# Performance work log

Hardware: AMD Instinct MI355X
Metric: run time of the kernel (lower is better)

## Reference

```python
import jax, jax.numpy as jnp
import numpy as np

NUM_EMB = 256
EMB_DIM = 32
B, N = 16, 16384
TEMPERATURE = 1.0      # current value of the temperature buffer
TEMP_MIN = 0.5
TEMP_INIT_REF = 2.0    # constant used in temp_ratio denominator in the torch code


def setup_inputs() -> dict:
    key = jax.random.key(0)
    k1, k2, k3 = jax.random.split(key, 3)
    inputs = jax.random.normal(k1, (B, N, EMB_DIM), dtype=jnp.float32)
    embedding = jax.random.normal(k2, (NUM_EMB, EMB_DIM), dtype=jnp.float32) * 0.1
    gumbel_u = jax.random.uniform(k3, (B * N, NUM_EMB), dtype=jnp.float32)
    return {"inputs": inputs, "embedding": embedding, "gumbel_u": gumbel_u}


def reference(inputs, embedding, gumbel_u):
    input_shape = inputs.shape
    flat = inputs.reshape(-1, EMB_DIM)                       # [M, D]

    distances = (jnp.sum(flat ** 2, axis=1, keepdims=True)
                 - 2.0 * jnp.matmul(flat, embedding.T)
                 + jnp.sum(embedding ** 2, axis=1))
    logits = -distances / TEMPERATURE

    # training branch: gumbel noise + softmax at temperature
    gumbel = -jnp.log(-jnp.log(gumbel_u + 1e-20) + 1e-20)
    soft = jax.nn.softmax((logits + gumbel) / TEMPERATURE, axis=-1)  # [M, K]

    quantized_soft = jnp.matmul(soft, embedding)             # [M, D]
    indices = jnp.argmax(soft, axis=-1)                      # [M]
    quantized_hard = embedding[indices]                      # [M, D]

    temp_ratio = (TEMPERATURE - TEMP_MIN) / (TEMP_INIT_REF - TEMP_MIN)
    quantized = temp_ratio * quantized_soft + (1.0 - temp_ratio) * quantized_hard
    # straight-through estimator
    quantized = flat + jax.lax.stop_gradient(quantized - flat)

    commitment_loss = jnp.mean((jax.lax.stop_gradient(quantized_hard) - flat) ** 2)

    avg_probs = jnp.mean(soft, axis=0)                       # [K]
    perplexity = jnp.exp(-jnp.sum(avg_probs * jnp.log(avg_probs + 1e-10)))

    quantized = quantized.reshape(input_shape)
    indices = indices.reshape(input_shape[:-1])
    return quantized, commitment_loss, indices, perplexity
```

## Files before the change

kernel.cpp:

```cpp
#include <hip/hip_runtime.h>


#define M_ROWS  262144
#define OUT_LOSS 8388608
#define OUT_IDX  8388609
#define OUT_PPL  8650753

#if defined(__has_builtin)
#if __has_builtin(__builtin_amdgcn_global_load_lds)
#define HAVE_GLLDS 1
#else
#define HAVE_GLLDS 0
#endif
#else
#define HAVE_GLLDS 0
#endif

typedef float f32x2 __attribute__((ext_vector_type(2)));

__device__ __forceinline__ f32x2 mk2(float a, float b) {
  f32x2 r; r.x = a; r.y = b; return r;
}

__device__ __forceinline__ unsigned int f2bf_u(float f) {
  unsigned int u = __float_as_uint(f);
  u += 0x7fffu + ((u >> 16) & 1u);
  return u >> 16;
}
__device__ __forceinline__ float bf2f(unsigned int lo16) {
  return __uint_as_float(lo16 << 16);
}

__global__ __launch_bounds__(256) void vq_prep(const float* __restrict__ emb,
                                               float* __restrict__ ws) {
  int t = threadIdx.x;
  ws[t] = 0.0f;
  if (t == 0) ws[256] = 0.0f;
  const float4* e4 = (const float4*)emb;
  float s = 0.0f;
#pragma unroll
  for (int j = 0; j < 8; ++j) {
    float4 v = e4[t * 8 + j];
    s += v.x * v.x + v.y * v.y + v.z * v.z + v.w * v.w;
  }
  ws[257 + t] = s;
}

__global__ __launch_bounds__(256, 4) void vq_pass1(
    const float* __restrict__ x_in, const float* __restrict__ emb,
    const float* __restrict__ gum,
    float* __restrict__ invS_ws, unsigned short* __restrict__ p_ws,
    float* __restrict__ loss_ws, float* __restrict__ out) {
  __shared__ __align__(16) float x_lds[16 * 36];
  __shared__ __align__(16) float g_lds[16 * 256];
  __shared__ float t_lds[256 * 17];
  __shared__ float red_sum[16 * 17];
  __shared__ float red_max[16 * 17];
  __shared__ int   red_idx[16 * 17];

  const int tid = threadIdx.x;
  const int wv  = tid >> 6;
  const int ln  = tid & 63;

  const float S2    = 2.8853900817779268f;
  const float L2E   = 1.4426950408889634f;
  const float GOFF  = 0.5287663729448977f;
  const float EPS2  = 1.4426950408889634e-20f;

  f32x2 er2[16];
  float ne_t;
  {
    const float4* e4 = (const float4*)(emb + tid * 32);
    float na = 0.0f;
#pragma unroll
    for (int j = 0; j < 8; ++j) {
      float4 v = e4[j];
      na = fmaf(v.x, v.x, na); na = fmaf(v.y, v.y, na);
      na = fmaf(v.z, v.z, na); na = fmaf(v.w, v.w, na);
      er2[2*j]   = mk2(v.x * S2, v.y * S2);
      er2[2*j+1] = mk2(v.z * S2, v.w * S2);
    }
    ne_t = na * L2E;
  }
  const int row_blk = blockIdx.x * 256;
  float cl_acc = 0.0f;

#if HAVE_GLLDS
  auto issue_g = [&](int ttn) {
    const char* gbase = (const char*)(gum + (size_t)(row_blk + ttn * 16) * 256);
#pragma unroll
    for (int i = 0; i < 4; ++i) {
      const int off = i * 4096 + wv * 1024;
      __builtin_amdgcn_global_load_lds(
          (const __attribute__((address_space(1))) void*)(gbase + off + ln * 16),
          (__attribute__((address_space(3))) void*)((char*)g_lds + off),
          16, 0, 0);
    }
  };
  issue_g(0);
#endif

  for (int tt = 0; tt < 16; ++tt) {
    const int r0 = row_blk + tt * 16;

#if !HAVE_GLLDS
    {
      const float4* gg = (const float4*)gum + (size_t)r0 * 64;
      float4* gd = (float4*)g_lds;
#pragma unroll
      for (int i = 0; i < 4; ++i) gd[i * 256 + tid] = gg[i * 256 + tid];
    }
#endif
    if (tid < 128)
      *((float4*)&x_lds[(tid >> 3) * 36 + (tid & 7) * 4]) =
          ((const float4*)x_in)[(size_t)r0 * 8 + tid];
    __syncthreads();

#pragma unroll 1
    for (int r = 0; r < 16; ++r) {
      const float u = g_lds[r * 256 + tid];
      const float L1 = __log2f(u + 1e-20f);
      const float gp = GOFF - __log2f(EPS2 - L1);
      const float4* xr4 = (const float4*)&x_lds[r * 36];
      f32x2 a0 = mk2(0.f, 0.f), a1 = mk2(0.f, 0.f);
#pragma unroll
      for (int j = 0; j < 8; ++j) {
        const float4 xv = xr4[j];
        a0 = __builtin_elementwise_fma(mk2(xv.x, xv.y), er2[2*j],   a0);
        a1 = __builtin_elementwise_fma(mk2(xv.z, xv.w), er2[2*j+1], a1);
      }
      const float dot2 = (a0.x + a1.x) + (a0.y + a1.y);
      t_lds[tid * 17 + r] = dot2 + (gp - ne_t);
    }
    __syncthreads();

#if HAVE_GLLDS
    if (tt < 15) issue_g(tt + 1);
#endif

    const int lrow = tid & 15;
    const int cs   = tid >> 4;
    {
      float ssum = 0.0f, tmax = -3.0e38f;
      int   kmax = 0;
      unsigned int packs[8];
#pragma unroll
      for (int j = 0; j < 16; ++j) {
        const int k = cs * 16 + j;
        const float tv = t_lds[k * 17 + lrow];
        const float p = exp2f(tv);
        ssum += p;
        if (tv > tmax) { tmax = tv; kmax = k; }
        if (j & 1) packs[j >> 1] |= f2bf_u(p) << 16;
        else       packs[j >> 1]  = f2bf_u(p);
      }
      uint4* pout = (uint4*)(p_ws + (size_t)(r0 + lrow) * 256 + cs * 16);
      const uint4* pd = (const uint4*)packs;
      pout[0] = pd[0]; pout[1] = pd[1];
      red_sum[lrow * 17 + cs] = ssum;
      red_max[lrow * 17 + cs] = tmax;
      red_idx[lrow * 17 + cs] = kmax;
    }
    __syncthreads();

    if (tid < 16) {
      float ssum = 0.0f, tmax = -3.0e38f;
      int   kmax = 0;
#pragma unroll
      for (int c = 0; c < 16; ++c) {
        ssum += red_sum[tid * 17 + c];
        const float m = red_max[tid * 17 + c];
        if (m > tmax) { tmax = m; kmax = red_idx[tid * 17 + c]; }
      }
      const int rg = r0 + tid;
      invS_ws[rg] = 1.0f / ssum;
      out[OUT_IDX + rg] = (float)kmax;

      const float4* eh = (const float4*)(emb + (size_t)kmax * 32);
      const float* xrr = &x_lds[tid * 36];
      float cl = 0.0f;
#pragma unroll
      for (int j = 0; j < 8; ++j) {
        const float4 e  = eh[j];
        const float4 xv = ((const float4*)xrr)[j];
        float dx;
        dx = e.x - xv.x; cl = fmaf(dx, dx, cl);
        dx = e.y - xv.y; cl = fmaf(dx, dx, cl);
        dx = e.z - xv.z; cl = fmaf(dx, dx, cl);
        dx = e.w - xv.w; cl = fmaf(dx, dx, cl);
      }
#pragma unroll
      for (int off = 8; off > 0; off >>= 1) cl += __shfl_down(cl, off, 16);
      if (tid == 0) cl_acc += cl;
    }
    __syncthreads();
  }
  if (tid == 0) atomicAdd(loss_ws, cl_acc);
}

__global__ __launch_bounds__(256, 4) void vq_pass2(
    const float* __restrict__ emb, const unsigned short* __restrict__ p_ws,
    const float* __restrict__ invS_ws, float* __restrict__ out) {
  __shared__ __align__(16) float e_lds[256 * 32];

  const int tid = threadIdx.x;
  {
    const float4* src = (const float4*)emb;
    float4* dst = (float4*)e_lds;
#pragma unroll
    for (int j = 0; j < 8; ++j) dst[j * 256 + tid] = src[j * 256 + tid];
  }
  __syncthreads();

  const int row = blockIdx.x * 256 + tid;
  const float invS = invS_ws[row];
  const int imax = (int)out[OUT_IDX + row];
  const uint4* pv = (const uint4*)(p_ws + (size_t)row * 256);
  const float4* el4 = (const float4*)e_lds;

  f32x2 q2[16];
#pragma unroll
  for (int d = 0; d < 16; ++d) q2[d] = mk2(0.f, 0.f);

  for (int kg = 0; kg < 8; ++kg) {
    unsigned int w_[16];
#pragma unroll
    for (int j = 0; j < 4; ++j) {
      const uint4 v = pv[kg * 4 + j];
      w_[4*j+0] = v.x; w_[4*j+1] = v.y; w_[4*j+2] = v.z; w_[4*j+3] = v.w;
    }
#pragma unroll
    for (int i = 0; i < 16; ++i) {
      const int k0 = kg * 32 + 2 * i;
      const f32x2 pp0 = mk2(bf2f(w_[i] & 0xffffu), bf2f(w_[i] & 0xffffu));
      const f32x2 pp1 = mk2(bf2f(w_[i] >> 16),     bf2f(w_[i] >> 16));
#pragma unroll
      for (int jj = 0; jj < 8; ++jj) {
        const float4 e0 = el4[k0 * 8 + jj];
        const float4 e1 = el4[(k0 + 1) * 8 + jj];
        q2[2*jj]   = __builtin_elementwise_fma(mk2(e0.x, e0.y), pp0, q2[2*jj]);
        q2[2*jj+1] = __builtin_elementwise_fma(mk2(e0.z, e0.w), pp0, q2[2*jj+1]);
        q2[2*jj]   = __builtin_elementwise_fma(mk2(e1.x, e1.y), pp1, q2[2*jj]);
        q2[2*jj+1] = __builtin_elementwise_fma(mk2(e1.z, e1.w), pp1, q2[2*jj+1]);
      }
    }
  }

  const float tr  = 1.0f / 3.0f;
  const float otr = 1.0f - tr;
  const float4* ehv = el4 + imax * 8;
  float4* outq = (float4*)(out + (size_t)row * 32);
#pragma unroll
  for (int j = 0; j < 8; ++j) {
    float4 e = ehv[j];
    float4 o;
    o.x = fmaf(tr, q2[2*j].x   * invS, otr * e.x);
    o.y = fmaf(tr, q2[2*j].y   * invS, otr * e.y);
    o.z = fmaf(tr, q2[2*j+1].x * invS, otr * e.z);
    o.w = fmaf(tr, q2[2*j+1].y * invS, otr * e.w);
    outq[j] = o;
  }
}

__global__ __launch_bounds__(256) void vq_avg(
    const unsigned short* __restrict__ p_ws, const float* __restrict__ invS_ws,
    float* __restrict__ avg_ws) {
  __shared__ float sh[256];
  const int tid = threadIdx.x, lane = tid & 63, w = tid >> 6;
  sh[tid] = 0.0f;
  __syncthreads();
  const int base = (blockIdx.x * 4 + w) * 64;
  const float iv = invS_ws[base + lane];
  float a0 = 0.f, a1 = 0.f, a2 = 0.f, a3 = 0.f;
  for (int r = 0; r < 64; ++r) {
    const float s = __shfl(iv, r);
    const uint2 u2 = ((const uint2*)(p_ws + (size_t)(base + r) * 256))[lane];
    a0 = fmaf(bf2f(u2.x & 0xffffu), s, a0);
    a1 = fmaf(bf2f(u2.x >> 16),     s, a1);
    a2 = fmaf(bf2f(u2.y & 0xffffu), s, a2);
    a3 = fmaf(bf2f(u2.y >> 16),     s, a3);
  }
  atomicAdd(&sh[4*lane+0], a0);
  atomicAdd(&sh[4*lane+1], a1);
  atomicAdd(&sh[4*lane+2], a2);
  atomicAdd(&sh[4*lane+3], a3);
  __syncthreads();
  atomicAdd(&avg_ws[tid], sh[tid]);
}

__global__ __launch_bounds__(256) void vq_fin(const float* __restrict__ ws,
                                              float* __restrict__ out) {
  __shared__ float red[256];
  int t = threadIdx.x;
  float avg = ws[t] * (1.0f / 262144.0f);
  red[t] = -avg * __logf(avg + 1e-10f);
  __syncthreads();
  for (int s = 128; s > 0; s >>= 1) {
    if (t < s) red[t] += red[t + s];
    __syncthreads();
  }
  if (t == 0) {
    out[OUT_PPL]  = __expf(red[0]);
    out[OUT_LOSS] = ws[256] * (1.0f / 8388608.0f);
  }
}

__global__ __launch_bounds__(256, 1) void vq_main(
    const float* __restrict__ x_in, const float* __restrict__ emb,
    const float* __restrict__ gum, const float* __restrict__ ne,
    float* __restrict__ avg_ws, float* __restrict__ loss_ws,
    float* __restrict__ out) {
  extern __shared__ unsigned char dynsmem[];
  unsigned short* p_lds = (unsigned short*)dynsmem;

  const int tid  = threadIdx.x;
  const int lane = tid & 63;
  const int w    = tid >> 6;
  const int row  = blockIdx.x * 256 + tid;
  unsigned short* my_p = p_lds + (size_t)(w * 64 + lane) * 258;

  float xr[32];
  {
    const float4* xv = (const float4*)(x_in + (size_t)row * 32);
#pragma unroll
    for (int j = 0; j < 8; ++j) {
      float4 v = xv[j];
      xr[4*j+0] = v.x; xr[4*j+1] = v.y; xr[4*j+2] = v.z; xr[4*j+3] = v.w;
    }
  }
  float q[32];
#pragma unroll
  for (int d = 0; d < 32; ++d) q[d] = 0.0f;

  float ssum = 0.0f;
  float tmax = -3.0e38f;
  int   imax = 0;

  const float4* g4 = (const float4*)(gum + (size_t)row * 256);
  const float4* e4 = (const float4*)emb;

  for (int kg = 0; kg < 8; ++kg) {
    float uv[32];
#pragma unroll
    for (int j = 0; j < 8; ++j) {
      float4 v = g4[kg * 8 + j];
      uv[4*j+0] = v.x; uv[4*j+1] = v.y; uv[4*j+2] = v.z; uv[4*j+3] = v.w;
    }
#pragma unroll
    for (int kk = 0; kk < 32; ++kk) {
      const int k = kg * 32 + kk;
      float er[32];
#pragma unroll
      for (int j = 0; j < 8; ++j) {
        float4 v = e4[k * 8 + j];
        er[4*j+0] = v.x; er[4*j+1] = v.y; er[4*j+2] = v.z; er[4*j+3] = v.w;
      }
      float d0 = 0.f, d1 = 0.f, d2 = 0.f, d3 = 0.f;
#pragma unroll
      for (int d = 0; d < 32; d += 4) {
        d0 = fmaf(xr[d+0], er[d+0], d0);
        d1 = fmaf(xr[d+1], er[d+1], d1);
        d2 = fmaf(xr[d+2], er[d+2], d2);
        d3 = fmaf(xr[d+3], er[d+3], d3);
      }
      const float dot = (d0 + d1) + (d2 + d3);
      const float inner = -__logf(uv[kk] + 1e-20f);
      const float g = -__logf(inner + 1e-20f);
      const float t = fmaf(2.0f, dot, g) - ne[k];
      const float p = __expf(t);
      ssum += p;
      if (t > tmax) { tmax = t; imax = k; }
#pragma unroll
      for (int d = 0; d < 32; ++d) q[d] = fmaf(p, er[d], q[d]);
      my_p[k] = (unsigned short)f2bf_u(p);
    }
  }

  const float invS = 1.0f / ssum;
  {
    const float tr  = 1.0f / 3.0f;
    const float otr = 1.0f - tr;
    const float4* ehv = (const float4*)(emb + (size_t)imax * 32);
    float4* outq = (float4*)(out + (size_t)row * 32);
    float cl = 0.0f;
#pragma unroll
    for (int j = 0; j < 8; ++j) {
      float4 e = ehv[j];
      float4 o;
      float qs, dx;
      qs = q[4*j+0]*invS; o.x = tr*qs + otr*e.x; dx = e.x - xr[4*j+0]; cl = fmaf(dx,dx,cl);
      qs = q[4*j+1]*invS; o.y = tr*qs + otr*e.y; dx = e.y - xr[4*j+1]; cl = fmaf(dx,dx,cl);
      qs = q[4*j+2]*invS; o.z = tr*qs + otr*e.z; dx = e.z - xr[4*j+2]; cl = fmaf(dx,dx,cl);
      qs = q[4*j+3]*invS; o.w = tr*qs + otr*e.w; dx = e.w - xr[4*j+3]; cl = fmaf(dx,dx,cl);
      outq[j] = o;
    }
    out[OUT_IDX + row] = (float)imax;
#pragma unroll
    for (int off = 32; off > 0; off >>= 1) cl += __shfl_down(cl, off);
    if (lane == 0) atomicAdd(loss_ws, cl);
  }

  __syncthreads();

  float a0 = 0.f, a1 = 0.f, a2 = 0.f, a3 = 0.f;
  for (int r = 0; r < 64; ++r) {
    const float invS_r = __shfl(invS, r);
    const unsigned short* rp = p_lds + (size_t)(w * 64 + r) * 258;
    a0 = fmaf(bf2f(rp[  0 + lane]), invS_r, a0);
    a1 = fmaf(bf2f(rp[ 64 + lane]), invS_r, a1);
    a2 = fmaf(bf2f(rp[128 + lane]), invS_r, a2);
    a3 = fmaf(bf2f(rp[192 + lane]), invS_r, a3);
  }
  atomicAdd(&avg_ws[  0 + lane], a0);
  atomicAdd(&avg_ws[ 64 + lane], a1);
  atomicAdd(&avg_ws[128 + lane], a2);
  atomicAdd(&avg_ws[192 + lane], a3);
}

extern "C" void kernel_launch(void* const* d_in, const int* in_sizes, int n_in,
                              void* d_out, int out_size, void* d_ws, size_t ws_size,
                              hipStream_t stream) {
  const float* x   = (const float*)d_in[0];
  const float* emb = (const float*)d_in[1];
  const float* gum = (const float*)d_in[2];
  float* out = (float*)d_out;
  float* ws  = (float*)d_ws;

  (void)in_sizes; (void)n_in; (void)out_size;

  vq_prep<<<1, 256, 0, stream>>>(emb, ws);

  const size_t need = (size_t)(1024 + M_ROWS) * 4 + (size_t)M_ROWS * 256 * 2;
  if (ws_size >= need) {
    float* invS = ws + 1024;
    unsigned short* p = (unsigned short*)(ws + 1024 + M_ROWS);
    vq_pass1<<<1024, 256, 0, stream>>>(x, emb, gum, invS, p, ws + 256, out);
    vq_pass2<<<1024, 256, 0, stream>>>(emb, p, invS, out);
    vq_avg<<<1024, 256, 0, stream>>>(p, invS, ws);
  } else {
    (void)hipFuncSetAttribute((const void*)vq_main,
                        hipFuncAttributeMaxDynamicSharedMemorySize, 132128);
    vq_main<<<1024, 256, 132128, stream>>>(x, emb, gum, ws + 257, ws, ws + 256, out);
  }
  vq_fin<<<1, 256, 0, stream>>>(ws, out);
}
```

Measured before the change: 262.3 us.

## Fuse codebook-usage averaging into pass1 and drop the separate avg kernel

Result: slower. 269.1 us (+2.6%).

```diff
diff --git a/kernel.cpp b/kernel.cpp
--- a/kernel.cpp
+++ b/kernel.cpp
@@ -50,13 +50,15 @@
     const float* __restrict__ x_in, const float* __restrict__ emb,
     const float* __restrict__ gum,
     float* __restrict__ invS_ws, unsigned short* __restrict__ p_ws,
-    float* __restrict__ loss_ws, float* __restrict__ out) {
+    float* __restrict__ loss_ws, float* __restrict__ avg_ws,
+    float* __restrict__ out) {
   __shared__ __align__(16) float x_lds[16 * 36];
   __shared__ __align__(16) float g_lds[16 * 256];
   __shared__ float t_lds[256 * 17];
   __shared__ float red_sum[16 * 17];
   __shared__ float red_max[16 * 17];
   __shared__ int   red_idx[16 * 17];
+  __shared__ float sh_invS[16];
 
   const int tid = threadIdx.x;
   const int wv  = tid >> 6;
@@ -83,7 +85,8 @@
     ne_t = na * L2E;
   }
   const int row_blk = blockIdx.x * 256;
-  float cl_acc = 0.0f;
+  float cl_acc  = 0.0f;
+  float avg_acc = 0.0f;
 
 #if HAVE_GLLDS
   auto issue_g = [&](int ttn) {
@@ -173,7 +176,9 @@
         if (m > tmax) { tmax = m; kmax = red_idx[tid * 17 + c]; }
       }
       const int rg = r0 + tid;
-      invS_ws[rg] = 1.0f / ssum;
+      const float iv = 1.0f / ssum;
+      invS_ws[rg] = iv;
+      sh_invS[tid] = iv;
       out[OUT_IDX + rg] = (float)kmax;
 
       const float4* eh = (const float4*)(emb + (size_t)kmax * 32);
@@ -194,8 +199,23 @@
       if (tid == 0) cl_acc += cl;
     }
     __syncthreads();
+
+    {
+      const float ivr = sh_invS[lrow];
+#pragma unroll
+      for (int j = 0; j < 16; ++j) {
+        const int k = cs * 16 + j;
+        float v = exp2f(t_lds[k * 17 + lrow]) * ivr;
+        v += __shfl_xor(v, 1, 64);
+        v += __shfl_xor(v, 2, 64);
+        v += __shfl_xor(v, 4, 64);
+        v += __shfl_xor(v, 8, 64);
+        if (lrow == j) avg_acc += v;
+      }
+    }
   }
   if (tid == 0) atomicAdd(loss_ws, cl_acc);
+  atomicAdd(&avg_ws[tid], avg_acc);
 }
 
 __global__ __launch_bounds__(256, 4) void vq_pass2(
@@ -260,32 +280,6 @@
     o.w = fmaf(tr, q2[2*j+1].y * invS, otr * e.w);
     outq[j] = o;
   }
-}
-
-__global__ __launch_bounds__(256) void vq_avg(
-    const unsigned short* __restrict__ p_ws, const float* __restrict__ invS_ws,
-    float* __restrict__ avg_ws) {
-  __shared__ float sh[256];
-  const int tid = threadIdx.x, lane = tid & 63, w = tid >> 6;
-  sh[tid] = 0.0f;
-  __syncthreads();
-  const int base = (blockIdx.x * 4 + w) * 64;
-  const float iv = invS_ws[base + lane];
-  float a0 = 0.f, a1 = 0.f, a2 = 0.f, a3 = 0.f;
-  for (int r = 0; r < 64; ++r) {
-    const float s = __shfl(iv, r);
-    const uint2 u2 = ((const uint2*)(p_ws + (size_t)(base + r) * 256))[lane];
-    a0 = fmaf(bf2f(u2.x & 0xffffu), s, a0);
-    a1 = fmaf(bf2f(u2.x >> 16),     s, a1);
-    a2 = fmaf(bf2f(u2.y & 0xffffu), s, a2);
-    a3 = fmaf(bf2f(u2.y >> 16),     s, a3);
-  }
-  atomicAdd(&sh[4*lane+0], a0);
-  atomicAdd(&sh[4*lane+1], a1);
-  atomicAdd(&sh[4*lane+2], a2);
-  atomicAdd(&sh[4*lane+3], a3);
-  __syncthreads();
-  atomicAdd(&avg_ws[tid], sh[tid]);
 }
 
 __global__ __launch_bounds__(256) void vq_fin(const float* __restrict__ ws,
@@ -434,9 +428,8 @@
   if (ws_size >= need) {
     float* invS = ws + 1024;
     unsigned short* p = (unsigned short*)(ws + 1024 + M_ROWS);
-    vq_pass1<<<1024, 256, 0, stream>>>(x, emb, gum, invS, p, ws + 256, out);
+    vq_pass1<<<1024, 256, 0, stream>>>(x, emb, gum, invS, p, ws + 256, ws, out);
     vq_pass2<<<1024, 256, 0, stream>>>(emb, p, invS, out);
-    vq_avg<<<1024, 256, 0, stream>>>(p, invS, ws);
   } else {
     (void)hipFuncSetAttribute((const void*)vq_main,
                         hipFuncAttributeMaxDynamicSharedMemorySize, 132128);
```
